# Performance work log

Measured on AMD Instinct MI355X. Metric: run time of the kernel, lower is better.

The kernel has to match this reference:

```python
import jax, jax.numpy as jnp
import numpy as np

D_MODEL = 2048
N_HEADS = 16
D_HEAD = 128
BATCH = 2
SEQ = 2048
INIT_STD = 0.02
N_LAYERS = 12


def setup_inputs() -> dict:
    key = jax.random.key(0)
    ks = jax.random.split(key, 5)
    attn_std = INIT_STD
    proj_std = INIT_STD / np.sqrt(2 * N_LAYERS)
    return {
        "normalized_resid_pre": jax.random.normal(ks[0], (BATCH, SEQ, D_MODEL), jnp.float32),
        "W_Q": jax.random.normal(ks[1], (N_HEADS, D_MODEL, D_HEAD), jnp.float32) * attn_std,
        "W_K": jax.random.normal(ks[2], (N_HEADS, D_MODEL, D_HEAD), jnp.float32) * attn_std,
        "W_V": jax.random.normal(ks[3], (N_HEADS, D_MODEL, D_HEAD), jnp.float32) * attn_std,
        "W_O": jax.random.normal(ks[4], (N_HEADS, D_HEAD, D_MODEL), jnp.float32) * proj_std,
        "b_Q": jnp.zeros((N_HEADS, D_HEAD), jnp.float32),
        "b_K": jnp.zeros((N_HEADS, D_HEAD), jnp.float32),
        "b_V": jnp.zeros((N_HEADS, D_HEAD), jnp.float32),
        "b_O": jnp.zeros((D_MODEL,), jnp.float32),
    }


def reference(normalized_resid_pre, W_Q, W_K, W_V, W_O, b_Q, b_K, b_V, b_O):
    x = normalized_resid_pre
    # q,k,v: [batch, posn, nheads, d_head]
    q = jnp.einsum('bsd,hde->bshe', x, W_Q) + b_Q
    k = jnp.einsum('bsd,hde->bshe', x, W_K) + b_K
    v = jnp.einsum('bsd,hde->bshe', x, W_V) + b_V
    # scores: [batch, nheads, posn_Q, posn_K]
    scores = jnp.einsum('bqhe,bkhe->bhqk', q, k) / jnp.sqrt(jnp.float32(D_HEAD))
    S = scores.shape[-1]
    causal = jnp.tril(jnp.ones((S, S), bool))
    scores = jnp.where(causal, scores, jnp.float32(-jnp.inf))
    pattern = jax.nn.softmax(scores, axis=-1)
    z = jnp.einsum('bhqk,bkhe->bqhe', pattern, v)
    attn_out = jnp.einsum('bqhe,hed->bqd', z, W_O) + b_O
    return attn_out
```

## Files before the change

### kernel.cpp

```cpp
#include <hip/hip_runtime.h>
#include <hip/hip_bf16.h>

typedef __hip_bfloat16 bf16;
typedef __attribute__((ext_vector_type(8))) short bf16x8;
typedef __attribute__((ext_vector_type(4))) short bf16x4;
typedef __attribute__((ext_vector_type(4))) float f32x4;

#define D_MODEL 2048
#define SEQ     2048
#define NH      16
#define DH      128
#define BATCH   2
#define MTOT    (BATCH*SEQ)

__device__ __forceinline__ void async_cp16(const bf16* g, bf16* l) {
    __builtin_amdgcn_global_load_lds(
        (const __attribute__((address_space(1))) void*)g,
        (__attribute__((address_space(3))) void*)l, 16, 0, 0);
}

__device__ __forceinline__ short bf16bits(float f) {
    bf16 b = __float2bfloat16(f);
    return *reinterpret_cast<short*>(&b);
}

#define GBAR() do { asm volatile("" ::: "memory"); __builtin_amdgcn_s_barrier(); \
                    asm volatile("" ::: "memory"); } while (0)

__global__ __launch_bounds__(256) void cvt_k(const float* __restrict__ in,
                                             bf16* __restrict__ out) {
    const long i = ((long)blockIdx.x * 256 + threadIdx.x) * 8;
    float4 a = *(const float4*)(in + i);
    float4 b = *(const float4*)(in + i + 4);
    __align__(16) bf16 t[8];
    t[0] = __float2bfloat16(a.x); t[1] = __float2bfloat16(a.y);
    t[2] = __float2bfloat16(a.z); t[3] = __float2bfloat16(a.w);
    t[4] = __float2bfloat16(b.x); t[5] = __float2bfloat16(b.y);
    t[6] = __float2bfloat16(b.z); t[7] = __float2bfloat16(b.w);
    *(bf16x8*)(out + i) = *(const bf16x8*)t;
}

__global__ __launch_bounds__(256) void transpose_cvt3_k(
    const float* __restrict__ in0, const float* __restrict__ in1,
    const float* __restrict__ in2,
    bf16* __restrict__ out, int R, int Cn, int mats_per_src)
{
    __shared__ float t[32][33];
    const int z = blockIdx.z;
    const int src = z / mats_per_src, mat = z % mats_per_src;
    const float* in = (src == 0) ? in0 : (src == 1) ? in1 : in2;
    const float* inm = in + (long)mat * R * Cn;
    bf16* outm = out + (long)z * R * Cn;
    const int c0 = blockIdx.x * 32, r0 = blockIdx.y * 32;
    const int tx = threadIdx.x & 31, ty = threadIdx.x >> 5;
#pragma unroll
    for (int i = 0; i < 4; ++i)
        t[ty + i*8][tx] = inm[(long)(r0 + ty + i*8) * Cn + c0 + tx];
    __syncthreads();
#pragma unroll
    for (int i = 0; i < 4; ++i)
        outm[(long)(c0 + ty + i*8) * R + r0 + tx] = __float2bfloat16(t[tx][ty + i*8]);
}

__global__ __launch_bounds__(256) void transpose_v_k(
    const bf16* __restrict__ V, bf16* __restrict__ VT)
{
    __shared__ bf16 t[32][33];
    const int bh = blockIdx.z;
    const int b = bh >> 4, h = bh & 15;
    const bf16* inm = V + (long)b*SEQ*D_MODEL + h*DH;
    bf16* outm = VT + (long)bh*DH*SEQ;
    const int r0 = blockIdx.x * 32;
    const int c0 = blockIdx.y * 32;
    const int tx = threadIdx.x & 31, ty = threadIdx.x >> 5;
#pragma unroll
    for (int i = 0; i < 4; ++i)
        t[ty + i*8][tx] = inm[(long)(r0 + ty + i*8)*D_MODEL + c0 + tx];
    __syncthreads();
#pragma unroll
    for (int i = 0; i < 4; ++i)
        outm[(long)(c0 + ty + i*8)*SEQ + r0 + tx] = t[tx][ty + i*8];
}

template <bool C_F32>
__device__ __forceinline__ void gemm128x128(
    const bf16* __restrict__ A, int lda,
    const bf16* __restrict__ Bt, int ldb,
    void* __restrict__ C, int ldc,
    const float* __restrict__ bias,
    int Kdim, int m0, int n0)
{
    __shared__ __align__(16) bf16 As[128*32];
    __shared__ __align__(16) bf16 Bs[128*32];
    const int tid  = threadIdx.x;
    const int wave = tid >> 6, lane = tid & 63;
    const int lr = lane & 15, lq = lane >> 4;
    const int wrow = wave >> 1, wcol = wave & 1;
    const int sr = lane >> 2, sk = (lane & 3) * 8;

    const f32x4 zero4 = {0.f, 0.f, 0.f, 0.f};
    f32x4 acc[4][4];
#pragma unroll
    for (int i = 0; i < 4; ++i)
#pragma unroll
        for (int j = 0; j < 4; ++j) acc[i][j] = zero4;

    for (int k0 = 0; k0 < Kdim; k0 += 32) {
#pragma unroll
        for (int c = 0; c < 2; ++c) {
            const int r = wave*32 + c*16;
            async_cp16(A  + (long)(m0 + r + sr)*lda + k0 + sk, As + r*32);
            async_cp16(Bt + (long)(n0 + r + sr)*ldb + k0 + sk, Bs + r*32);
        }
        __syncthreads();
        bf16x8 af[4], bfr[4];
#pragma unroll
        for (int i = 0; i < 4; ++i)
            af[i] = *(const bf16x8*)(As + (wrow*64 + i*16 + lr)*32 + lq*8);
#pragma unroll
        for (int j = 0; j < 4; ++j)
            bfr[j] = *(const bf16x8*)(Bs + (wcol*64 + j*16 + lr)*32 + lq*8);
#pragma unroll
        for (int i = 0; i < 4; ++i)
#pragma unroll
            for (int j = 0; j < 4; ++j)
                acc[i][j] = __builtin_amdgcn_mfma_f32_16x16x32_bf16(af[i], bfr[j], acc[i][j], 0, 0, 0);
        __syncthreads();
    }
#pragma unroll
    for (int j = 0; j < 4; ++j) {
        const int col = n0 + wcol*64 + j*16 + lr;
        const float bv = bias[col];
#pragma unroll
        for (int i = 0; i < 4; ++i) {
            const int row = m0 + wrow*64 + i*16 + lq*4;
#pragma unroll
            for (int r = 0; r < 4; ++r) {
                const float v = acc[i][j][r] + bv;
                if constexpr (C_F32) ((float*)C)[(long)(row + r)*ldc + col] = v;
                else ((bf16*)C)[(long)(row + r)*ldc + col] = __float2bfloat16(v);
            }
        }
    }
}

__global__ __launch_bounds__(256) void out_gemm_k(
    const bf16* __restrict__ Z, const bf16* __restrict__ WOT,
    const float* __restrict__ bO, float* __restrict__ Out)
{
    gemm128x128<true>(Z, D_MODEL, WOT, D_MODEL, Out, D_MODEL, bO, D_MODEL,
                      (int)blockIdx.x*128, (int)blockIdx.y*128);
}

__global__ __launch_bounds__(512) void qkv_gemm_k2(
    const bf16* __restrict__ A, const bf16* __restrict__ Bt,
    const float* __restrict__ bQ, const float* __restrict__ bK, const float* __restrict__ bV,
    bf16* __restrict__ Qo, bf16* __restrict__ Ko, bf16* __restrict__ Vo)
{
    __shared__ __align__(16) bf16 lds[36864];
    bf16* As = lds;
    bf16* Bs = lds + 12288;

    const int lin = blockIdx.x;
    const int xcd = lin & 7, idx = lin >> 3;
    const int m0 = (idx & 31) * 128;
    const int n0 = (xcd * 3 + (idx >> 5)) * 256;

    const int tid = threadIdx.x, wave = tid >> 6, lane = tid & 63;
    const int wm = wave >> 2, wn = wave & 3;
    const int lr = lane & 15, lq = lane >> 4;
    const int sph = (lr >> 1) & 3;

    const int s_r  = lane >> 2;
    const int s_sl = lane & 3;

    auto stageA = [&](int t, int slot) {
        const int k = t * 32;
        const int r = wave*16 + s_r;
        async_cp16(A + (long)(m0 + r)*D_MODEL + k + ((s_sl ^ ((r >> 1) & 3)) * 8),
                   As + slot*4096 + wave*512);
    };
    auto stageB = [&](int t, int slot) {
        const int k = t * 32;
#pragma unroll
        for (int i = 0; i < 2; ++i) {
            const int c = wave*2 + i;
            const int r = c*16 + s_r;
            async_cp16(Bt + (long)(n0 + r)*D_MODEL + k + ((s_sl ^ ((r >> 1) & 3)) * 8),
                       Bs + slot*8192 + c*512);
        }
    };
    auto rdA = [&](int slot, int fm) -> bf16x8 {
        const int r = wm*64 + fm*16 + lr;
        return *(const bf16x8*)(As + slot*4096 + r*32 + ((lq ^ sph) * 8));
    };
    auto rdB = [&](int slot, int fn) -> bf16x8 {
        const int r = wn*64 + fn*16 + lr;
        return *(const bf16x8*)(Bs + slot*8192 + r*32 + ((lq ^ sph) * 8));
    };

    const f32x4 zero4 = {0.f, 0.f, 0.f, 0.f};
    f32x4 acc[4][4];
#pragma unroll
    for (int i = 0; i < 4; ++i)
#pragma unroll
        for (int j = 0; j < 4; ++j) acc[i][j] = zero4;

    const int NT = D_MODEL / 32;

    stageA(0, 0); stageB(0, 0);
    stageA(1, 1); stageB(1, 1);
    asm volatile("s_waitcnt vmcnt(3)" ::: "memory");
    GBAR();

    int cur = 0, s2 = 2;
    for (int t = 0; t < NT; ++t) {
        bf16x8 aF[4], bF[4];
#pragma unroll
        for (int j = 0; j < 4; ++j) aF[j] = rdA(cur, j);
#pragma unroll
        for (int j = 0; j < 4; ++j) bF[j] = rdB(cur, j);
        if (t + 2 < NT) { stageA(t + 2, s2); stageB(t + 2, s2); }

        __builtin_amdgcn_s_setprio(1);
#pragma unroll
        for (int fm = 0; fm < 4; ++fm)
#pragma unroll
            for (int fn = 0; fn < 4; ++fn)
                acc[fm][fn] = __builtin_amdgcn_mfma_f32_16x16x32_bf16(aF[fm], bF[fn], acc[fm][fn], 0, 0, 0);
        __builtin_amdgcn_s_setprio(0);

        if (t + 2 < NT) asm volatile("s_waitcnt vmcnt(3)" ::: "memory");
        else            asm volatile("s_waitcnt vmcnt(0)" ::: "memory");
        GBAR();

        cur = (cur == 2) ? 0 : cur + 1;
        s2  = (s2  == 2) ? 0 : s2  + 1;
    }

    const int gc0 = n0 + wn*64;
    const int sel = gc0 >> 11;
    bf16* C        = (sel == 0) ? Qo : (sel == 1) ? Ko : Vo;
    const float* bs = (sel == 0) ? bQ : (sel == 1) ? bK : bV;
#pragma unroll
    for (int fn = 0; fn < 4; ++fn) {
        const int dcol = (gc0 + fn*16 + lr) & 2047;
        const float bv = bs[dcol];
#pragma unroll
        for (int fm = 0; fm < 4; ++fm) {
            const int row = m0 + wm*64 + fm*16 + lq*4;
#pragma unroll
            for (int rr = 0; rr < 4; ++rr)
                C[(long)(row + rr)*D_MODEL + dcol] = __float2bfloat16(acc[fm][fn][rr] + bv);
        }
    }
}

__global__ __launch_bounds__(512) void flash_k(
    const bf16* __restrict__ Q, const bf16* __restrict__ K,
    const bf16* __restrict__ VT, bf16* __restrict__ Z)
{
    __shared__ __align__(16) bf16 Ks[64*128];
    __shared__ __align__(16) bf16 Vts[128*64];
    __shared__ __align__(16) bf16 Ps[128*72];

    const int qt = (int)(gridDim.x - 1) - (int)blockIdx.x;
    const int bh = blockIdx.y;
    const int b  = bh >> 4, h = bh & 15;
    const long base = (long)b*SEQ*D_MODEL + h*DH;
    const bf16* Qb  = Q + base;
    const bf16* Kb  = K + base;
    const bf16* VTb = VT + (long)bh*DH*SEQ;
    bf16* Zb = Z + base;
    const int q0 = qt*128;
    const int tid = threadIdx.x, wave = tid >> 6, lane = tid & 63;
    const int lr = lane & 15, lq = lane >> 4;
    const int rx = lr & 7;

    const int ks_key_off = lane >> 4;
    const int ks_slot    = lane & 15;
    const int vt_row_off = lane >> 3;
    const int vt_slot    = lane & 7;

    bf16x8 aq[4];
#pragma unroll
    for (int ks = 0; ks < 4; ++ks)
        aq[ks] = *(const bf16x8*)(Qb + (long)(q0 + wave*16 + lr)*D_MODEL + ks*32 + lq*8);

    const f32x4 zero4 = {0.f, 0.f, 0.f, 0.f};
    f32x4 o_acc[8];
#pragma unroll
    for (int jf = 0; jf < 8; ++jf) o_acc[jf] = zero4;
    float m_run = -1e30f, l_run = 0.f;

    const float scale = 0.08838834764831845f;
    const int NT = 2*qt + 2;

    for (int kt = 0; kt < NT; ++kt) {
        const int k0 = kt*64;
        __syncthreads();
#pragma unroll
        for (int c2 = 0; c2 < 2; ++c2) {
            const int c = wave*2 + c2;
            const int key = c*4 + ks_key_off;
            async_cp16(Kb + (long)(k0 + key)*D_MODEL + ((ks_slot ^ (key & 7)) * 8),
                       Ks + c*512);
            const int f = c*8 + vt_row_off;
            async_cp16(VTb + (long)f*SEQ + k0 + ((vt_slot ^ (f & 7)) * 8),
                       Vts + c*512);
        }
        __syncthreads();

        const int rel_hi = q0 + wave*16 + 15 - k0;
        if (rel_hi >= 0) {
            f32x4 sc[4];
#pragma unroll
            for (int mt = 0; mt < 4; ++mt) sc[mt] = zero4;
            __builtin_amdgcn_s_setprio(1);
#pragma unroll
            for (int mt = 0; mt < 4; ++mt)
#pragma unroll
                for (int ks = 0; ks < 4; ++ks) {
                    bf16x8 bk = *(const bf16x8*)(Ks + (mt*16 + lr)*128 + (((ks*4 + lq) ^ rx) * 8));
                    sc[mt] = __builtin_amdgcn_mfma_f32_16x16x32_bf16(bk, aq[ks], sc[mt], 0, 0, 0);
                }
            __builtin_amdgcn_s_setprio(0);

            if (rel_hi < 78) {
                const int rel = q0 + wave*16 + lr - k0;
#pragma unroll
                for (int mt = 0; mt < 4; ++mt)
#pragma unroll
                    for (int r = 0; r < 4; ++r)
                        if (mt*16 + lq*4 + r > rel) sc[mt][r] = -1e30f;
            }

            float mx = sc[0][0];
#pragma unroll
            for (int mt = 0; mt < 4; ++mt)
#pragma unroll
                for (int r = 0; r < 4; ++r) mx = fmaxf(mx, sc[mt][r]);
            mx = fmaxf(mx, __shfl_xor(mx, 16, 64));
            mx = fmaxf(mx, __shfl_xor(mx, 32, 64));
            mx *= scale;

            if (!__all(mx - m_run <= 8.0f)) {
                const float mn = fmaxf(m_run, mx);
                const float al = __expf(m_run - mn);
                l_run *= al;
#pragma unroll
                for (int jf = 0; jf < 8; ++jf)
#pragma unroll
                    for (int r = 0; r < 4; ++r) o_acc[jf][r] *= al;
                m_run = mn;
            }

            float rs = 0.f;
#pragma unroll
            for (int mt = 0; mt < 4; ++mt)
#pragma unroll
                for (int r = 0; r < 4; ++r) {
                    const float p = __expf(fmaf(sc[mt][r], scale, -m_run));
                    sc[mt][r] = p;
                    rs += p;
                }
            rs += __shfl_xor(rs, 16, 64);
            rs += __shfl_xor(rs, 32, 64);
            l_run += rs;

#pragma unroll
            for (int mt = 0; mt < 4; ++mt) {
                bf16x4 pk;
#pragma unroll
                for (int r = 0; r < 4; ++r) pk[r] = bf16bits(sc[mt][r]);
                *(bf16x4*)(Ps + (wave*16 + lr)*72 + mt*16 + lq*4) = pk;
            }

            bf16x8 pb0 = *(const bf16x8*)(Ps + (wave*16 + lr)*72 + lq*8);
            bf16x8 pb1 = *(const bf16x8*)(Ps + (wave*16 + lr)*72 + 32 + lq*8);

            __builtin_amdgcn_s_setprio(1);
#pragma unroll
            for (int jf = 0; jf < 8; ++jf) {
                const int f = jf*16 + lr;
                bf16x8 av0 = *(const bf16x8*)(Vts + f*64 + ((lq ^ rx) * 8));
                bf16x8 av1 = *(const bf16x8*)(Vts + f*64 + (((4 + lq) ^ rx) * 8));
                o_acc[jf] = __builtin_amdgcn_mfma_f32_16x16x32_bf16(av0, pb0, o_acc[jf], 0, 0, 0);
                o_acc[jf] = __builtin_amdgcn_mfma_f32_16x16x32_bf16(av1, pb1, o_acc[jf], 0, 0, 0);
            }
            __builtin_amdgcn_s_setprio(0);
        }
    }

    const float inv = 1.f / l_run;
    const long zrow = (long)(q0 + wave*16 + lr) * D_MODEL;
#pragma unroll
    for (int jf = 0; jf < 8; ++jf) {
        bf16x4 pk;
#pragma unroll
        for (int r = 0; r < 4; ++r) pk[r] = bf16bits(o_acc[jf][r] * inv);
        *(bf16x4*)(Zb + zrow + jf*16 + lq*4) = pk;
    }
}

extern "C" void kernel_launch(void* const* d_in, const int* in_sizes, int n_in,
                              void* d_out, int out_size, void* d_ws, size_t ws_size,
                              hipStream_t stream) {
    const float* X  = (const float*)d_in[0];
    const float* WQ = (const float*)d_in[1];
    const float* WK = (const float*)d_in[2];
    const float* WV = (const float*)d_in[3];
    const float* WO = (const float*)d_in[4];
    const float* bQ = (const float*)d_in[5];
    const float* bK = (const float*)d_in[6];
    const float* bV = (const float*)d_in[7];
    const float* bO = (const float*)d_in[8];
    float* out = (float*)d_out;

    bf16* ws = (bf16*)d_ws;
    const long WSZ = (long)NH*DH*D_MODEL;
    const long MSZ = (long)MTOT*D_MODEL;
    bf16* Xb  = ws;
    bf16* WT3 = Xb + MSZ;
    bf16* WOT = WT3 + 3*WSZ;
    bf16* Qb  = WOT + WSZ;
    bf16* Kb  = Qb + MSZ;
    bf16* Vb  = Kb + MSZ;
    bf16* Zb  = Xb;
    bf16* VT  = WT3;

    cvt_k<<<MSZ/(256*8), 256, 0, stream>>>(X, Xb);
    transpose_cvt3_k<<<dim3(DH/32, D_MODEL/32, 3*NH), 256, 0, stream>>>(
        WQ, WK, WV, WT3, D_MODEL, DH, NH);
    transpose_cvt3_k<<<dim3(D_MODEL/32, D_MODEL/32, 1), 256, 0, stream>>>(
        WO, WO, WO, WOT, D_MODEL, D_MODEL, 1);

    qkv_gemm_k2<<<dim3((MTOT/128)*(3*D_MODEL/256)), 512, 0, stream>>>(
        Xb, WT3, bQ, bK, bV, Qb, Kb, Vb);
    transpose_v_k<<<dim3(SEQ/32, DH/32, BATCH*NH), 256, 0, stream>>>(Vb, VT);
    flash_k<<<dim3(SEQ/128, BATCH*NH), 512, 0, stream>>>(Qb, Kb, VT, Zb);
    out_gemm_k<<<dim3(MTOT/128, D_MODEL/128), 256, 0, stream>>>(Zb, WOT, bO, out);
}
```

Before: 408.0 us.

## Replace output GEMM with triple-buffered swizzled 128x256 kernel; add early barrier

Swaps the simple single-buffered 128x128 output-projection GEMM for a copy of the QKV GEMM design. The new kernel uses 512 threads, a 128x256 tile, three-slot async LDS staging, XOR-swizzled LDS addressing and XCD-aware block mapping. The aim is to overlap global loads with MFMA work, cut the per-K-step double __syncthreads stalls and reduce LDS bank conflicts. It also adds an extra block barrier plus an lgkmcnt wait and a sched_barrier before the MFMA loop in both GEMMs, which makes the fragment reads explicit but adds a sync per iteration.

```diff
diff --git a/kernel.cpp b/kernel.cpp
--- a/kernel.cpp
+++ b/kernel.cpp
@@ -82,75 +82,6 @@
         outm[(long)(c0 + ty + i*8)*SEQ + r0 + tx] = t[tx][ty + i*8];
 }
 
-template <bool C_F32>
-__device__ __forceinline__ void gemm128x128(
-    const bf16* __restrict__ A, int lda,
-    const bf16* __restrict__ Bt, int ldb,
-    void* __restrict__ C, int ldc,
-    const float* __restrict__ bias,
-    int Kdim, int m0, int n0)
-{
-    __shared__ __align__(16) bf16 As[128*32];
-    __shared__ __align__(16) bf16 Bs[128*32];
-    const int tid  = threadIdx.x;
-    const int wave = tid >> 6, lane = tid & 63;
-    const int lr = lane & 15, lq = lane >> 4;
-    const int wrow = wave >> 1, wcol = wave & 1;
-    const int sr = lane >> 2, sk = (lane & 3) * 8;
-
-    const f32x4 zero4 = {0.f, 0.f, 0.f, 0.f};
-    f32x4 acc[4][4];
-#pragma unroll
-    for (int i = 0; i < 4; ++i)
-#pragma unroll
-        for (int j = 0; j < 4; ++j) acc[i][j] = zero4;
-
-    for (int k0 = 0; k0 < Kdim; k0 += 32) {
-#pragma unroll
-        for (int c = 0; c < 2; ++c) {
-            const int r = wave*32 + c*16;
-            async_cp16(A  + (long)(m0 + r + sr)*lda + k0 + sk, As + r*32);
-            async_cp16(Bt + (long)(n0 + r + sr)*ldb + k0 + sk, Bs + r*32);
-        }
-        __syncthreads();
-        bf16x8 af[4], bfr[4];
-#pragma unroll
-        for (int i = 0; i < 4; ++i)
-            af[i] = *(const bf16x8*)(As + (wrow*64 + i*16 + lr)*32 + lq*8);
-#pragma unroll
-        for (int j = 0; j < 4; ++j)
-            bfr[j] = *(const bf16x8*)(Bs + (wcol*64 + j*16 + lr)*32 + lq*8);
-#pragma unroll
-        for (int i = 0; i < 4; ++i)
-#pragma unroll
-            for (int j = 0; j < 4; ++j)
-                acc[i][j] = __builtin_amdgcn_mfma_f32_16x16x32_bf16(af[i], bfr[j], acc[i][j], 0, 0, 0);
-        __syncthreads();
-    }
-#pragma unroll
-    for (int j = 0; j < 4; ++j) {
-        const int col = n0 + wcol*64 + j*16 + lr;
-        const float bv = bias[col];
-#pragma unroll
-        for (int i = 0; i < 4; ++i) {
-            const int row = m0 + wrow*64 + i*16 + lq*4;
-#pragma unroll
-            for (int r = 0; r < 4; ++r) {
-                const float v = acc[i][j][r] + bv;
-                if constexpr (C_F32) ((float*)C)[(long)(row + r)*ldc + col] = v;
-                else ((bf16*)C)[(long)(row + r)*ldc + col] = __float2bfloat16(v);
-            }
-        }
-    }
-}
-
-__global__ __launch_bounds__(256) void out_gemm_k(
-    const bf16* __restrict__ Z, const bf16* __restrict__ WOT,
-    const float* __restrict__ bO, float* __restrict__ Out)
-{
-    gemm128x128<true>(Z, D_MODEL, WOT, D_MODEL, Out, D_MODEL, bO, D_MODEL,
-                      (int)blockIdx.x*128, (int)blockIdx.y*128);
-}
 
 __global__ __launch_bounds__(512) void qkv_gemm_k2(
     const bf16* __restrict__ A, const bf16* __restrict__ Bt,
@@ -170,7 +101,6 @@
     const int wm = wave >> 2, wn = wave & 3;
     const int lr = lane & 15, lq = lane >> 4;
     const int sph = (lr >> 1) & 3;
-
     const int s_r  = lane >> 2;
     const int s_sl = lane & 3;
 
@@ -222,6 +152,10 @@
         for (int j = 0; j < 4; ++j) bF[j] = rdB(cur, j);
         if (t + 2 < NT) { stageA(t + 2, s2); stageB(t + 2, s2); }
 
+        GBAR();
+        asm volatile("s_waitcnt lgkmcnt(0)" ::: "memory");
+        __builtin_amdgcn_sched_barrier(0);
+
         __builtin_amdgcn_s_setprio(1);
 #pragma unroll
         for (int fm = 0; fm < 4; ++fm)
@@ -252,6 +186,109 @@
 #pragma unroll
             for (int rr = 0; rr < 4; ++rr)
                 C[(long)(row + rr)*D_MODEL + dcol] = __float2bfloat16(acc[fm][fn][rr] + bv);
+        }
+    }
+}
+
+__global__ __launch_bounds__(512) void out_gemm_k2(
+    const bf16* __restrict__ A, const bf16* __restrict__ Bt,
+    const float* __restrict__ bO, float* __restrict__ Out)
+{
+    __shared__ __align__(16) bf16 lds[36864];
+    bf16* As = lds;
+    bf16* Bs = lds + 12288;
+
+    const int lin = blockIdx.x;
+    const int xcd = lin & 7, idx = lin >> 3;
+    const int m0 = idx * 128;
+    const int n0 = xcd * 256;
+
+    const int tid = threadIdx.x, wave = tid >> 6, lane = tid & 63;
+    const int wm = wave >> 2, wn = wave & 3;
+    const int lr = lane & 15, lq = lane >> 4;
+    const int sph = (lr >> 1) & 3;
+    const int s_r  = lane >> 2;
+    const int s_sl = lane & 3;
+
+    auto stageA = [&](int t, int slot) {
+        const int k = t * 32;
+        const int r = wave*16 + s_r;
+        async_cp16(A + (long)(m0 + r)*D_MODEL + k + ((s_sl ^ ((r >> 1) & 3)) * 8),
+                   As + slot*4096 + wave*512);
+    };
+    auto stageB = [&](int t, int slot) {
+        const int k = t * 32;
+#pragma unroll
+        for (int i = 0; i < 2; ++i) {
+            const int c = wave*2 + i;
+            const int r = c*16 + s_r;
+            async_cp16(Bt + (long)(n0 + r)*D_MODEL + k + ((s_sl ^ ((r >> 1) & 3)) * 8),
+                       Bs + slot*8192 + c*512);
+        }
+    };
+    auto rdA = [&](int slot, int fm) -> bf16x8 {
+        const int r = wm*64 + fm*16 + lr;
+        return *(const bf16x8*)(As + slot*4096 + r*32 + ((lq ^ sph) * 8));
+    };
+    auto rdB = [&](int slot, int fn) -> bf16x8 {
+        const int r = wn*64 + fn*16 + lr;
+        return *(const bf16x8*)(Bs + slot*8192 + r*32 + ((lq ^ sph) * 8));
+    };
+
+    const f32x4 zero4 = {0.f, 0.f, 0.f, 0.f};
+    f32x4 acc[4][4];
+#pragma unroll
+    for (int i = 0; i < 4; ++i)
+#pragma unroll
+        for (int j = 0; j < 4; ++j) acc[i][j] = zero4;
+
+    const int NT = D_MODEL / 32;
+
+    stageA(0, 0); stageB(0, 0);
+    stageA(1, 1); stageB(1, 1);
+    asm volatile("s_waitcnt vmcnt(3)" ::: "memory");
+    GBAR();
+
+    int cur = 0, s2 = 2;
+    for (int t = 0; t < NT; ++t) {
+        bf16x8 aF[4], bF[4];
+#pragma unroll
+        for (int j = 0; j < 4; ++j) aF[j] = rdA(cur, j);
+#pragma unroll
+        for (int j = 0; j < 4; ++j) bF[j] = rdB(cur, j);
+        if (t + 2 < NT) { stageA(t + 2, s2); stageB(t + 2, s2); }
+
+        GBAR();
+        asm volatile("s_waitcnt lgkmcnt(0)" ::: "memory");
+        __builtin_amdgcn_sched_barrier(0);
+
+        __builtin_amdgcn_s_setprio(1);
+#pragma unroll
+        for (int fm = 0; fm < 4; ++fm)
+#pragma unroll
+            for (int fn = 0; fn < 4; ++fn)
+                acc[fm][fn] = __builtin_amdgcn_mfma_f32_16x16x32_bf16(aF[fm], bF[fn], acc[fm][fn], 0, 0, 0);
+        __builtin_amdgcn_s_setprio(0);
+
+        if (t + 2 < NT) asm volatile("s_waitcnt vmcnt(3)" ::: "memory");
+        else            asm volatile("s_waitcnt vmcnt(0)" ::: "memory");
+        GBAR();
+
+        cur = (cur == 2) ? 0 : cur + 1;
+        s2  = (s2  == 2) ? 0 : s2  + 1;
+    }
+
+    const int gc0 = n0 + wn*64;
+#pragma unroll
+    for (int fn = 0; fn < 4; ++fn) {
+        const int col = gc0 + fn*16 + lr;
+        const float bv = bO[col];
+#pragma unroll
+        for (int fm = 0; fm < 4; ++fm) {
+            const int row = m0 + wm*64 + fm*16 + lq*4;
+#pragma unroll
+            for (int rr = 0; rr < 4; ++rr)
+                Out[(long)(row + rr)*D_MODEL + col] = acc[fm][fn][rr] + bv;
         }
     }
 }
@@ -439,5 +476,5 @@
         Xb, WT3, bQ, bK, bV, Qb, Kb, Vb);
     transpose_v_k<<<dim3(SEQ/32, DH/32, BATCH*NH), 256, 0, stream>>>(Vb, VT);
     flash_k<<<dim3(SEQ/128, BATCH*NH), 512, 0, stream>>>(Qb, Kb, VT, Zb);
-    out_gemm_k<<<dim3(MTOT/128, D_MODEL/128), 256, 0, stream>>>(Zb, WOT, bO, out);
-}
+    out_gemm_k2<<<dim3((MTOT/128)*(D_MODEL/256)), 512, 0, stream>>>(Zb, WOT, bO, out);
+}
```

After: 396.0 us. -2.9%, faster.
